# Kernel optimization log

Measured on AMD Instinct MI355X. Metric: run time of the kernel, lower is better.

The kernel has to match this reference:

```python
import jax, jax.numpy as jnp
import numpy as np

HEADS = 16


def setup_inputs() -> dict:
    key = jax.random.key(0)
    ks = jax.random.split(key, 6)
    b, n, c = 4, 2048, 1024  # batch, seq_len, query_dim (== hidden_dim)
    h = 1024                 # hidden_dim = heads * dim_head = 16 * 64
    s = 0.02
    return {
        "x": jax.random.normal(ks[0], (b, n, c), jnp.float32),
        "Wq": jax.random.normal(ks[1], (h, c), jnp.float32) * s,
        "Wk": jax.random.normal(ks[2], (h, c), jnp.float32) * s,
        "Wv": jax.random.normal(ks[3], (h, c), jnp.float32) * s,
        "Wout": jax.random.normal(ks[4], (c, h), jnp.float32) * s,
        "bout": jnp.zeros((c,), jnp.float32),
    }


def reference(x, Wq, Wk, Wv, Wout, bout):
    # x: (b, n, c). Self-attention (context = x).
    b, n, c = x.shape
    m = HEADS
    d = Wq.shape[0] // m  # dim_head
    # 1x1 conv == linear projection over channel dim
    q = jnp.einsum('bnc,hc->bnh', x, Wq).reshape(b, n, m, d)
    k = jnp.einsum('bnc,hc->bnh', x, Wk).reshape(b, n, m, d)
    v = jnp.einsum('bnc,hc->bnh', x, Wv).reshape(b, n, m, d)
    scale = d ** (-0.25)  # 1/sqrt(sqrt(d)), applied to both q and k
    # weight: (b, m, n_q, n_k)
    weight = jnp.einsum('bimd,bjmd->bmij', q * scale, k * scale)
    weight = jax.nn.softmax(weight, axis=-1)
    a = jnp.einsum('bmij,bjmd->bimd', weight, v).reshape(b, n, m * d)
    return jnp.einsum('bnh,ch->bnc', a, Wout) + bout
```

## Files before the change

kernel.cpp:

```cpp
#include <hip/hip_runtime.h>
#include <stdint.h>
#include <stddef.h>

typedef __attribute__((ext_vector_type(4))) float f32x4;
typedef __attribute__((ext_vector_type(16))) float f32x16;
typedef __attribute__((ext_vector_type(8))) short s16x8;
typedef __attribute__((ext_vector_type(4))) short s16x4;
typedef __attribute__((ext_vector_type(2))) int i32x2;

__device__ __forceinline__ short f2bf(float f) {
  uint32_t u = __builtin_bit_cast(uint32_t, f);
  uint32_t r = (u + 0x7fffu + ((u >> 16) & 1u)) >> 16;
  return (short)r;
}

__device__ __forceinline__ void gload_lds16(const void* g, void* l) {
  __builtin_amdgcn_global_load_lds(
      (const __attribute__((address_space(1))) void*)g,
      (__attribute__((address_space(3))) void*)l, 16, 0, 0);
}

__device__ __forceinline__ int msk8(int r) { return (r & 7) ^ ((r >> 3) & 7); }
__device__ __forceinline__ int swz(int r, int c) {
  return r * 64 + (c ^ (msk8(r) << 3));
}

__global__ __launch_bounds__(256) void cvt_kernel(const float* __restrict__ src,
                                                  short* __restrict__ dst, int n4) {
  int i = blockIdx.x * blockDim.x + threadIdx.x;
  if (i >= n4) return;
  float4 v = reinterpret_cast<const float4*>(src)[i];
  s16x4 o;
  o[0] = f2bf(v.x); o[1] = f2bf(v.y); o[2] = f2bf(v.z); o[3] = f2bf(v.w);
  reinterpret_cast<s16x4*>(dst)[i] = o;
}

template <int OUTF32>
__global__ __launch_bounds__(256) void gemm_bt(const short* __restrict__ A,
                                               const short* __restrict__ B,
                                               void* __restrict__ Cv,
                                               const float* __restrict__ bias,
                                               int M, int N, int K,
                                               float qscl, int qcols) {
  __shared__ short lA[128 * 64];
  __shared__ short lB[128 * 64];
  const int tid = threadIdx.x;
  const int lane = tid & 63, wid = tid >> 6;
  const int g = lane >> 4, li = lane & 15;
  const int nbx = N >> 7;
  const int q8 = gridDim.x >> 3;
  const int orig = blockIdx.x;
  const int bswz = (orig & 7) * q8 + (orig >> 3);
  const int by = bswz / nbx, bx = bswz % nbx;
  const int brow = by << 7, bcol = bx << 7;
  const int wr = (wid >> 1) << 6, wc = (wid & 1) << 6;

  f32x4 acc[4][4] = {};

  for (int k0 = 0; k0 < K; k0 += 64) {
    __syncthreads();
#pragma unroll
    for (int i = 0; i < 4; i++) {
      int j = tid + i * 256;
      int r = j >> 3, s = j & 7;
      gload_lds16(A + (size_t)(brow + r) * K + k0 + 8 * (s ^ msk8(r)), &lA[j * 8]);
    }
#pragma unroll
    for (int i = 0; i < 4; i++) {
      int j = tid + i * 256;
      int r = j >> 3, s = j & 7;
      gload_lds16(B + (size_t)(bcol + r) * K + k0 + 8 * (s ^ msk8(r)), &lB[j * 8]);
    }
    __syncthreads();
#pragma unroll
    for (int ks = 0; ks < 2; ks++) {
      s16x8 af[4], bfr[4];
#pragma unroll
      for (int ai = 0; ai < 4; ai++) {
        int row = wr + ai * 16 + li;
        af[ai] = *(const s16x8*)&lA[swz(row, ks * 32 + g * 8)];
      }
#pragma unroll
      for (int bj = 0; bj < 4; bj++) {
        int row = wc + bj * 16 + li;
        bfr[bj] = *(const s16x8*)&lB[swz(row, ks * 32 + g * 8)];
      }
#pragma unroll
      for (int ai = 0; ai < 4; ai++)
#pragma unroll
        for (int bj = 0; bj < 4; bj++)
          acc[ai][bj] = __builtin_amdgcn_mfma_f32_16x16x32_bf16(af[ai], bfr[bj],
                                                               acc[ai][bj], 0, 0, 0);
    }
  }

#pragma unroll
  for (int ai = 0; ai < 4; ai++) {
#pragma unroll
    for (int bj = 0; bj < 4; bj++) {
#pragma unroll
      for (int e = 0; e < 4; e++) {
        int row = brow + wr + ai * 16 + g * 4 + e;
        int col = bcol + wc + bj * 16 + li;
        float v = acc[ai][bj][e];
        if (col < qcols) v *= qscl;
        if (OUTF32) {
          ((float*)Cv)[(size_t)row * N + col] = v + bias[col];
        } else {
          ((short*)Cv)[(size_t)row * N + col] = f2bf(v);
        }
      }
    }
  }
}

__global__ __launch_bounds__(256, 4) void attn_kernel(const short* __restrict__ qkv,
                                                      short* __restrict__ aout) {
  __shared__ short lds[2][8192];

  const int tid = threadIdx.x;
  const int lane = tid & 63, w = tid >> 6;
  const int l31 = lane & 31, hi = lane >> 5;
  const int bid = blockIdx.x;
  const int qt = bid & 15, head = (bid >> 4) & 15, b = bid >> 8;
  const int row0 = b * 2048;
  const int qrow = qt * 128 + w * 32 + l31;
  const int qcol = head * 64, kcol = 1024 + head * 64, vcol = 2048 + head * 64;

#pragma unroll
  for (int s = 0; s < 4; s++)
    gload_lds16(qkv + (size_t)(row0 + qrow) * 3072 + qcol + 16 * s + 8 * hi,
                &lds[0][(w * 4 + s) * 512]);
  __syncthreads();
  s16x8 qf[4];
#pragma unroll
  for (int s = 0; s < 4; s++)
    qf[s] = *(const s16x8*)&lds[0][(w * 4 + s) * 512 + lane * 8];
  __syncthreads();

  const int vj = tid >> 3, va = tid & 7;
  const int vdd = va >> 2, va3 = va & 3;
  const int vhi = (vj >> 3) & 1, vks = vj >> 4, vef = vj & 7;
  const int vblk = (vks * 2 + vdd) * 512;
  const int vxor = va3 | (vhi << 2);
  const int vslot_r = (lane ^ ((lane >> 3) & 7)) * 8;

#pragma unroll
  for (int sub = 0; sub < 2; sub++)
    gload_lds16(qkv + (size_t)(row0 + sub * 32 + l31) * 3072 + kcol + 16 * w + 8 * hi,
                &lds[0][(sub * 4 + w) * 512]);
#pragma unroll
  for (int sub = 0; sub < 2; sub++) {
    s16x8 v0 = *(const s16x8*)(qkv + (size_t)(row0 + sub * 32 + vj) * 3072 + vcol + 8 * va);
#pragma unroll
    for (int t2 = 0; t2 < 8; t2++) {
      int slot = 32 * vhi + 8 * va3 + (t2 ^ vxor);
      lds[0][4096 + sub * 2048 + vblk + slot * 8 + vef] = v0[t2];
    }
  }
  __syncthreads();

  f32x16 acc0 = {}, acc1 = {};
  float m2 = -1e30f, l_r = 0.f;
  const float THR = 8.f * 1.44269504088896f;

  for (int jt = 0; jt < 32; jt++) {
    const int cur = jt & 1, nxt = cur ^ 1;
    const int jnext = (jt + 1) * 64;
    const bool pf = (jt < 31);

    s16x8 vs0, vs1;
    if (pf) {
      vs0 = *(const s16x8*)(qkv + (size_t)(row0 + jnext + vj) * 3072 + vcol + 8 * va);
      vs1 = *(const s16x8*)(qkv + (size_t)(row0 + jnext + 32 + vj) * 3072 + vcol + 8 * va);
#pragma unroll
      for (int sub = 0; sub < 2; sub++)
        gload_lds16(qkv + (size_t)(row0 + jnext + sub * 32 + l31) * 3072 + kcol +
                        16 * w + 8 * hi,
                    &lds[nxt][(sub * 4 + w) * 512]);
    }

    f32x16 st0 = {}, st1 = {};
    const short* lc = &lds[cur][0];
#pragma unroll
    for (int s = 0; s < 4; s++) {
      s16x8 kf0 = *(const s16x8*)&lc[s * 512 + lane * 8];
      s16x8 kf1 = *(const s16x8*)&lc[(4 + s) * 512 + lane * 8];
      st0 = __builtin_amdgcn_mfma_f32_32x32x16_bf16(kf0, qf[s], st0, 0, 0, 0);
      st1 = __builtin_amdgcn_mfma_f32_32x32x16_bf16(kf1, qf[s], st1, 0, 0, 0);
    }

    float pm = fmaxf(st0[0], st0[1]);
#pragma unroll
    for (int r = 2; r < 16; r++) pm = fmaxf(pm, st0[r]);
#pragma unroll
    for (int r = 0; r < 16; r++) pm = fmaxf(pm, st1[r]);
    pm = fmaxf(pm, __shfl_xor(pm, 32, 64));
    if (__any(pm > m2 + THR)) {
      float mn = fmaxf(m2, pm);
      float al = exp2f(m2 - mn);
      m2 = mn;
      l_r *= al;
#pragma unroll
      for (int r = 0; r < 16; r++) { acc0[r] *= al; acc1[r] *= al; }
    }
    float rs = 0.f;
#pragma unroll
    for (int r = 0; r < 16; r++) { st0[r] = exp2f(st0[r] - m2); rs += st0[r]; }
#pragma unroll
    for (int r = 0; r < 16; r++) { st1[r] = exp2f(st1[r] - m2); rs += st1[r]; }
    rs += __shfl_xor(rs, 32, 64);
    l_r += rs;

    if (pf) {
#pragma unroll
      for (int t2 = 0; t2 < 8; t2++) {
        int slot = 32 * vhi + 8 * va3 + (t2 ^ vxor);
        lds[nxt][4096 + vblk + slot * 8 + vef] = vs0[t2];
        lds[nxt][4096 + 2048 + vblk + slot * 8 + vef] = vs1[t2];
      }
    }

    const short* lV = &lds[cur][4096];
#pragma unroll
    for (int sub = 0; sub < 2; sub++) {
      const float* p = sub ? (const float*)&st1 : (const float*)&st0;
#pragma unroll
      for (int ks = 0; ks < 2; ks++) {
        int x0, x1, y0, y1;
        asm("v_cvt_pk_bf16_f32 %0, %1, %2" : "=v"(x0) : "v"(p[8*ks+0]), "v"(p[8*ks+1]));
        asm("v_cvt_pk_bf16_f32 %0, %1, %2" : "=v"(x1) : "v"(p[8*ks+2]), "v"(p[8*ks+3]));
        asm("v_cvt_pk_bf16_f32 %0, %1, %2" : "=v"(y0) : "v"(p[8*ks+4]), "v"(p[8*ks+5]));
        asm("v_cvt_pk_bf16_f32 %0, %1, %2" : "=v"(y1) : "v"(p[8*ks+6]), "v"(p[8*ks+7]));
        i32x2 s02 = __builtin_amdgcn_permlane32_swap(x0, y0, false, false);
        i32x2 s13 = __builtin_amdgcn_permlane32_swap(x1, y1, false, false);
        int4 paw; paw.x = s02[0]; paw.y = s13[0]; paw.z = s02[1]; paw.w = s13[1];
        s16x8 pa = __builtin_bit_cast(s16x8, paw);
        s16x8 v0 = *(const s16x8*)&lV[sub * 2048 + (ks * 2 + 0) * 512 + vslot_r];
        s16x8 v1 = *(const s16x8*)&lV[sub * 2048 + (ks * 2 + 1) * 512 + vslot_r];
        acc0 = __builtin_amdgcn_mfma_f32_32x32x16_bf16(v0, pa, acc0, 0, 0, 0);
        acc1 = __builtin_amdgcn_mfma_f32_32x32x16_bf16(v1, pa, acc1, 0, 0, 0);
      }
    }

    __syncthreads();
  }

  float inv = 1.f / l_r;
  const size_t rowoff = (size_t)(row0 + qt * 128 + w * 32 + l31) * 1024 + head * 64;
#pragma unroll
  for (int r = 0; r < 16; r++) {
    int dbase = (r & 3) + 8 * (r >> 2) + 4 * hi;
    aout[rowoff + dbase] = f2bf(acc0[r] * inv);
    aout[rowoff + 32 + dbase] = f2bf(acc1[r] * inv);
  }
}

extern "C" void kernel_launch(void* const* d_in, const int* in_sizes, int n_in,
                              void* d_out, int out_size, void* d_ws, size_t ws_size,
                              hipStream_t stream) {
  const float* x    = (const float*)d_in[0];
  const float* Wq   = (const float*)d_in[1];
  const float* Wk   = (const float*)d_in[2];
  const float* Wv   = (const float*)d_in[3];
  const float* Wout = (const float*)d_in[4];
  const float* bout = (const float*)d_in[5];
  float* out = (float*)d_out;

  char* ws = (char*)d_ws;
  short* xb    = (short*)(ws);
  short* Wqkv  = (short*)(ws + (16ull << 20));
  short* Woutb = (short*)(ws + (22ull << 20));
  short* qkv   = (short*)(ws + (24ull << 20));
  short* a_ws  = xb;

  const float SCL = 0.125f * 1.44269504088896f;

  cvt_kernel<<<8192, 256, 0, stream>>>(x, xb, 2097152);
  cvt_kernel<<<1024, 256, 0, stream>>>(Wq, Wqkv, 262144);
  cvt_kernel<<<1024, 256, 0, stream>>>(Wk, Wqkv + 1048576, 262144);
  cvt_kernel<<<1024, 256, 0, stream>>>(Wv, Wqkv + 2097152, 262144);
  cvt_kernel<<<1024, 256, 0, stream>>>(Wout, Woutb, 262144);

  gemm_bt<0><<<64 * 24, 256, 0, stream>>>(xb, Wqkv, qkv, nullptr, 8192, 3072, 1024,
                                          SCL, 1024);

  attn_kernel<<<1024, 256, 0, stream>>>(qkv, a_ws);

  gemm_bt<1><<<64 * 8, 256, 0, stream>>>(a_ws, Woutb, out, bout, 8192, 1024, 1024,
                                         1.f, 0);
}
```

Measured before the change: 300.3 us.

## Fuse weight conversions, relayout V in LDS to drop permlane swaps, add setprio

Merges the four weight-conversion launches into one kernel, which removes launch overhead. It changes the V tile layout in LDS so the P operand can be fed to the MFMA directly, dropping the permlane32 swaps. It also wraps the MFMA sections in s_setprio, restructures the max and sum reductions as vector trees, and vectorises the output stores to 4-wide. The new V swizzle risks LDS bank conflicts and is a correctness risk if the layout mapping is wrong.

```diff
diff --git a/kernel.cpp b/kernel.cpp
--- a/kernel.cpp
+++ b/kernel.cpp
@@ -6,7 +6,6 @@
 typedef __attribute__((ext_vector_type(16))) float f32x16;
 typedef __attribute__((ext_vector_type(8))) short s16x8;
 typedef __attribute__((ext_vector_type(4))) short s16x4;
-typedef __attribute__((ext_vector_type(2))) int i32x2;
 
 __device__ __forceinline__ short f2bf(float f) {
   uint32_t u = __builtin_bit_cast(uint32_t, f);
@@ -24,6 +23,7 @@
 __device__ __forceinline__ int swz(int r, int c) {
   return r * 64 + (c ^ (msk8(r) << 3));
 }
+__device__ __forceinline__ int swv(int d) { return d ^ ((d >> 3) & 3); }
 
 __global__ __launch_bounds__(256) void cvt_kernel(const float* __restrict__ src,
                                                   short* __restrict__ dst, int n4) {
@@ -33,6 +33,22 @@
   s16x4 o;
   o[0] = f2bf(v.x); o[1] = f2bf(v.y); o[2] = f2bf(v.z); o[3] = f2bf(v.w);
   reinterpret_cast<s16x4*>(dst)[i] = o;
+}
+
+__global__ __launch_bounds__(256) void cvt_w(const float* __restrict__ Wq,
+                                             const float* __restrict__ Wk,
+                                             const float* __restrict__ Wv,
+                                             const float* __restrict__ Wout,
+                                             short* __restrict__ Wqkv,
+                                             short* __restrict__ Woutb) {
+  int i = blockIdx.x * 256 + threadIdx.x;
+  int g = i >> 18, li = i & 262143;
+  const float* src = g == 0 ? Wq : g == 1 ? Wk : g == 2 ? Wv : Wout;
+  short* dst = g < 3 ? Wqkv + (size_t)g * 1048576 : Woutb;
+  float4 v = reinterpret_cast<const float4*>(src)[li];
+  s16x4 o;
+  o[0] = f2bf(v.x); o[1] = f2bf(v.y); o[2] = f2bf(v.z); o[3] = f2bf(v.w);
+  reinterpret_cast<s16x4*>(dst)[li] = o;
 }
 
 template <int OUTF32>
@@ -139,11 +155,12 @@
   __syncthreads();
 
   const int vj = tid >> 3, va = tid & 7;
-  const int vdd = va >> 2, va3 = va & 3;
-  const int vhi = (vj >> 3) & 1, vks = vj >> 4, vef = vj & 7;
-  const int vblk = (vks * 2 + vdd) * 512;
-  const int vxor = va3 | (vhi << 2);
-  const int vslot_r = (lane ^ ((lane >> 3) & 7)) * 8;
+  const int vks = vj >> 4;
+  const int vphi = (vj >> 2) & 1;
+  const int veV = (vj & 3) + 4 * ((vj >> 3) & 1);
+  const int vdd = va >> 2, va3 = va & 7 & 3;
+  const int vbase = (vks * 2 + vdd) * 512 + vphi * 256 + va3 * 64 + veV;
+  const int vslot_r = (32 * hi + swv(l31)) * 8;
 
 #pragma unroll
   for (int sub = 0; sub < 2; sub++)
@@ -153,10 +170,8 @@
   for (int sub = 0; sub < 2; sub++) {
     s16x8 v0 = *(const s16x8*)(qkv + (size_t)(row0 + sub * 32 + vj) * 3072 + vcol + 8 * va);
 #pragma unroll
-    for (int t2 = 0; t2 < 8; t2++) {
-      int slot = 32 * vhi + 8 * va3 + (t2 ^ vxor);
-      lds[0][4096 + sub * 2048 + vblk + slot * 8 + vef] = v0[t2];
-    }
+    for (int t2 = 0; t2 < 8; t2++)
+      lds[0][4096 + sub * 2048 + vbase + 8 * (t2 ^ va3)] = v0[t2];
   }
   __syncthreads();
 
@@ -182,6 +197,7 @@
 
     f32x16 st0 = {}, st1 = {};
     const short* lc = &lds[cur][0];
+    __builtin_amdgcn_s_setprio(1);
 #pragma unroll
     for (int s = 0; s < 4; s++) {
       s16x8 kf0 = *(const s16x8*)&lc[s * 512 + lane * 8];
@@ -189,52 +205,63 @@
       st0 = __builtin_amdgcn_mfma_f32_32x32x16_bf16(kf0, qf[s], st0, 0, 0, 0);
       st1 = __builtin_amdgcn_mfma_f32_32x32x16_bf16(kf1, qf[s], st1, 0, 0, 0);
     }
-
-    float pm = fmaxf(st0[0], st0[1]);
-#pragma unroll
-    for (int r = 2; r < 16; r++) pm = fmaxf(pm, st0[r]);
-#pragma unroll
-    for (int r = 0; r < 16; r++) pm = fmaxf(pm, st1[r]);
+    __builtin_amdgcn_s_setprio(0);
+
+    f32x16 mx;
+#pragma unroll
+    for (int r = 0; r < 16; r++) mx[r] = fmaxf(st0[r], st1[r]);
+    float pm = fmaxf(mx[0], mx[1]);
+#pragma unroll
+    for (int r = 2; r < 16; r += 2) pm = fmaxf(fmaxf(pm, mx[r]), mx[r + 1]);
     pm = fmaxf(pm, __shfl_xor(pm, 32, 64));
     if (__any(pm > m2 + THR)) {
       float mn = fmaxf(m2, pm);
       float al = exp2f(m2 - mn);
       m2 = mn;
       l_r *= al;
-#pragma unroll
-      for (int r = 0; r < 16; r++) { acc0[r] *= al; acc1[r] *= al; }
-    }
+      acc0 *= al;
+      acc1 *= al;
+    }
+    st0 = st0 - m2;
+    st1 = st1 - m2;
+#pragma unroll
+    for (int r = 0; r < 16; r++) st0[r] = exp2f(st0[r]);
+#pragma unroll
+    for (int r = 0; r < 16; r++) st1[r] = exp2f(st1[r]);
+    f32x16 sm = st0 + st1;
     float rs = 0.f;
 #pragma unroll
-    for (int r = 0; r < 16; r++) { st0[r] = exp2f(st0[r] - m2); rs += st0[r]; }
-#pragma unroll
-    for (int r = 0; r < 16; r++) { st1[r] = exp2f(st1[r] - m2); rs += st1[r]; }
+    for (int r = 0; r < 8; r++) sm[r] = sm[r] + sm[r + 8];
+#pragma unroll
+    for (int r = 0; r < 4; r++) sm[r] = sm[r] + sm[r + 4];
+    rs = (sm[0] + sm[1]) + (sm[2] + sm[3]);
     rs += __shfl_xor(rs, 32, 64);
     l_r += rs;
 
     if (pf) {
+      short* dst = &lds[nxt][4096];
 #pragma unroll
       for (int t2 = 0; t2 < 8; t2++) {
-        int slot = 32 * vhi + 8 * va3 + (t2 ^ vxor);
-        lds[nxt][4096 + vblk + slot * 8 + vef] = vs0[t2];
-        lds[nxt][4096 + 2048 + vblk + slot * 8 + vef] = vs1[t2];
+        int off = vbase + 8 * (t2 ^ va3);
+        dst[off] = vs0[t2];
+        dst[2048 + off] = vs1[t2];
       }
     }
 
     const short* lV = &lds[cur][4096];
+    __builtin_amdgcn_s_setprio(1);
 #pragma unroll
     for (int sub = 0; sub < 2; sub++) {
-      const float* p = sub ? (const float*)&st1 : (const float*)&st0;
+      const f32x16& pp = sub ? st1 : st0;
 #pragma unroll
       for (int ks = 0; ks < 2; ks++) {
-        int x0, x1, y0, y1;
-        asm("v_cvt_pk_bf16_f32 %0, %1, %2" : "=v"(x0) : "v"(p[8*ks+0]), "v"(p[8*ks+1]));
-        asm("v_cvt_pk_bf16_f32 %0, %1, %2" : "=v"(x1) : "v"(p[8*ks+2]), "v"(p[8*ks+3]));
-        asm("v_cvt_pk_bf16_f32 %0, %1, %2" : "=v"(y0) : "v"(p[8*ks+4]), "v"(p[8*ks+5]));
-        asm("v_cvt_pk_bf16_f32 %0, %1, %2" : "=v"(y1) : "v"(p[8*ks+6]), "v"(p[8*ks+7]));
-        i32x2 s02 = __builtin_amdgcn_permlane32_swap(x0, y0, false, false);
-        i32x2 s13 = __builtin_amdgcn_permlane32_swap(x1, y1, false, false);
-        int4 paw; paw.x = s02[0]; paw.y = s13[0]; paw.z = s02[1]; paw.w = s13[1];
+        int w0, w1, w2, w3;
+        asm("v_cvt_pk_bf16_f32 %0, %1, %2" : "=v"(w0) : "v"(pp[8*ks+0]), "v"(pp[8*ks+1]));
+        asm("v_cvt_pk_bf16_f32 %0, %1, %2" : "=v"(w1) : "v"(pp[8*ks+2]), "v"(pp[8*ks+3]));
+        asm("v_cvt_pk_bf16_f32 %0, %1, %2" : "=v"(w2) : "v"(pp[8*ks+4]), "v"(pp[8*ks+5]));
+        asm("v_cvt_pk_bf16_f32 %0, %1, %2" : "=v"(w3) : "v"(pp[8*ks+6]), "v"(pp[8*ks+7]));
+        int4 paw;
+        paw.x = w0; paw.y = w1; paw.z = w2; paw.w = w3;
         s16x8 pa = __builtin_bit_cast(s16x8, paw);
         s16x8 v0 = *(const s16x8*)&lV[sub * 2048 + (ks * 2 + 0) * 512 + vslot_r];
         s16x8 v1 = *(const s16x8*)&lV[sub * 2048 + (ks * 2 + 1) * 512 + vslot_r];
@@ -242,6 +269,7 @@
         acc1 = __builtin_amdgcn_mfma_f32_32x32x16_bf16(v1, pa, acc1, 0, 0, 0);
       }
     }
+    __builtin_amdgcn_s_setprio(0);
 
     __syncthreads();
   }
@@ -249,10 +277,16 @@
   float inv = 1.f / l_r;
   const size_t rowoff = (size_t)(row0 + qt * 128 + w * 32 + l31) * 1024 + head * 64;
 #pragma unroll
-  for (int r = 0; r < 16; r++) {
-    int dbase = (r & 3) + 8 * (r >> 2) + 4 * hi;
-    aout[rowoff + dbase] = f2bf(acc0[r] * inv);
-    aout[rowoff + 32 + dbase] = f2bf(acc1[r] * inv);
+  for (int rq = 0; rq < 4; rq++) {
+    s16x4 o0, o1;
+#pragma unroll
+    for (int i2 = 0; i2 < 4; i2++) {
+      o0[i2] = f2bf(acc0[rq * 4 + i2] * inv);
+      o1[i2] = f2bf(acc1[rq * 4 + i2] * inv);
+    }
+    int dbase = 8 * rq + 4 * hi;
+    *(s16x4*)&aout[rowoff + dbase] = o0;
+    *(s16x4*)&aout[rowoff + 32 + dbase] = o1;
   }
 }
 
@@ -277,10 +311,7 @@
   const float SCL = 0.125f * 1.44269504088896f;
 
   cvt_kernel<<<8192, 256, 0, stream>>>(x, xb, 2097152);
-  cvt_kernel<<<1024, 256, 0, stream>>>(Wq, Wqkv, 262144);
-  cvt_kernel<<<1024, 256, 0, stream>>>(Wk, Wqkv + 1048576, 262144);
-  cvt_kernel<<<1024, 256, 0, stream>>>(Wv, Wqkv + 2097152, 262144);
-  cvt_kernel<<<1024, 256, 0, stream>>>(Wout, Woutb, 262144);
+  cvt_w<<<4096, 256, 0, stream>>>(Wq, Wk, Wv, Wout, Wqkv, Woutb);
 
   gemm_bt<0><<<64 * 24, 256, 0, stream>>>(xb, Wqkv, qkv, nullptr, 8192, 3072, 1024,
                                           SCL, 1024);
```

New measurement: 303.5 us. Within noise of the previous version (+1.1%).
